# Optimization experiments

Hardware: AMD Instinct MI355X
Metric: run time of the kernel (lower is better)

The kernel has to match this reference:

```python
import jax, jax.numpy as jnp
import numpy as np

N = 50000      # nodes
E = 500000     # directed edges
F_IN = 112     # node feature dim
G = 256        # number of graphs in batch


def _lin(key, fan_in, fan_out):
    # torch nn.Linear default init: U(-1/sqrt(fan_in), 1/sqrt(fan_in))
    s = 1.0 / np.sqrt(fan_in)
    kw, kb = jax.random.split(key)
    W = jax.random.uniform(kw, (fan_in, fan_out), jnp.float32, -s, s)
    b = jax.random.uniform(kb, (fan_out,), jnp.float32, -s, s)
    return W, b


def setup_inputs() -> dict:
    key = jax.random.key(0)
    ks = jax.random.split(key, 9)
    x = jax.random.normal(ks[0], (N, F_IN), jnp.float32)
    edge_index = jax.random.randint(ks[1], (2, E), 0, N)
    # sorted graph ids, guaranteeing every graph id 0..G-1 appears
    batch = jnp.sort(jnp.concatenate([jnp.arange(G),
                                      jax.random.randint(ks[2], (N - G,), 0, G)]))
    W1, b1 = _lin(ks[3], F_IN, 336)
    W2, b2 = _lin(ks[4], 336, 168)
    Wg, bg = _lin(ks[5], 168, 84)
    Wf, bf = _lin(ks[6], 84, 42)
    Wo, bo = _lin(ks[7], 42, 1)
    return dict(x=x, edge_index=edge_index, batch=batch,
                W1=W1, b1=b1, W2=W2, b2=b2,
                Wg=Wg, bg=bg, Wf=Wf, bf=bf, Wo=Wo, bo=bo)


def _gcn_conv(x, W, b, src, dst, n):
    """PyG GCNConv: add self-loops, symmetric D^-1/2 A D^-1/2 normalization."""
    h = x @ W                                   # [n, out]
    loop = jnp.arange(n, dtype=src.dtype)
    src_f = jnp.concatenate([src, loop])        # [E+n]
    dst_f = jnp.concatenate([dst, loop])
    deg = jax.ops.segment_sum(jnp.ones(src_f.shape[0], jnp.float32), dst_f, n)
    dinv = jnp.where(deg > 0, jax.lax.rsqrt(deg), 0.0)
    norm = dinv[src_f] * dinv[dst_f]            # [E+n]
    out = jax.ops.segment_sum(h[src_f] * norm[:, None], dst_f, n)
    return out + b


def reference(x, edge_index, batch, W1, b1, W2, b2, Wg, bg, Wf, bf, Wo, bo):
    src, dst = edge_index[0], edge_index[1]
    h = jax.nn.relu(_gcn_conv(x, W1, b1, src, dst, N))
    # dropout is identity in eval mode
    h = jax.nn.relu(_gcn_conv(h, W2, b2, src, dst, N))
    g = jax.ops.segment_max(h, batch, G)        # global max pool -> [G, 168]
    g = jax.nn.relu(g @ Wg + bg)
    g = jax.nn.relu(g @ Wf + bf)
    return g @ Wo + bo                           # [G, 1]
```

## Files before the change

kernel.cpp:

```cpp
#include <hip/hip_runtime.h>
#include <hip/hip_fp16.h>

#define N_NODES 50000
#define MPAD    50048
#define N_EDGES 500000
#define F_IN    112
#define K1X     112
#define K1P     128
#define F1      336
#define K2P     352
#define F2      168
#define NGRAPH  256
#define SCAN_CHUNK 1024
#define SCAN_BLOCKS ((N_NODES + SCAN_CHUNK - 1) / SCAN_CHUNK)

typedef __attribute__((ext_vector_type(8))) _Float16 f16x8;
typedef __attribute__((ext_vector_type(4))) float f32x4;
typedef unsigned short ushort_t;

__device__ __forceinline__ ushort_t f16_bits(float x) {
    __half h = __float2half_rn(x);
    return *(ushort_t*)&h;
}

__global__ void k_zero_int(int* p, int n) {
    int i = blockIdx.x * blockDim.x + threadIdx.x;
    if (i < n) p[i] = 0;
}

#define CVX_ELEMS  (N_NODES * 28)
#define CVX_BLOCKS ((CVX_ELEMS + 255) / 256)
#define CNT_BLOCKS  ((N_EDGES / 2 + 255) / 256)
#define CVW1_BLOCKS ((384 * K1P + 255) / 256)
#define CVW2_BLOCKS ((192 * K2P + 255) / 256)
#define PREP_BLOCKS (CVX_BLOCKS + CNT_BLOCKS + CVW1_BLOCKS + CVW2_BLOCKS)

__global__ __launch_bounds__(256) void k_prep(const float* __restrict__ x,
                                              const int* __restrict__ dst,
                                              const float* __restrict__ W1,
                                              const float* __restrict__ W2,
                                              ushort_t* __restrict__ x16,
                                              int* __restrict__ dcount,
                                              ushort_t* __restrict__ w1t,
                                              ushort_t* __restrict__ w2t) {
    int bid = blockIdx.x;
    int t = threadIdx.x;
    if (bid < CVX_BLOCKS) {
        int i = bid * 256 + t;
        if (i < CVX_ELEMS) {
            float4 f = ((const float4*)x)[i];
            __half2 h0 = __floats2half2_rn(f.x, f.y);
            __half2 h1 = __floats2half2_rn(f.z, f.w);
            uint2 u; u.x = *(unsigned*)&h0; u.y = *(unsigned*)&h1;
            ((uint2*)x16)[i] = u;
        }
        return;
    }
    bid -= CVX_BLOCKS;
    if (bid < CNT_BLOCKS) {
        int i = bid * 256 + t;
        if (i < N_EDGES / 2) {
            int2 d = ((const int2*)dst)[i];
            atomicAdd(&dcount[d.x], 1);
            atomicAdd(&dcount[d.y], 1);
        }
        return;
    }
    bid -= CNT_BLOCKS;
    if (bid < CVW1_BLOCKS) {
        int idx = bid * 256 + t;
        if (idx < 384 * K1P) {
            int n = idx / K1P, k = idx % K1P;
            float v = (n < F1 && k < F_IN) ? W1[k * F1 + n] : 0.0f;
            w1t[idx] = f16_bits(v);
        }
        return;
    }
    bid -= CVW1_BLOCKS;
    {
        int idx = bid * 256 + t;
        if (idx < 192 * K2P) {
            int n = idx / K2P, k = idx % K2P;
            float v = (n < F2 && k < F1) ? W2[k * F2 + n] : 0.0f;
            w2t[idx] = f16_bits(v);
        }
    }
}

__global__ __launch_bounds__(SCAN_CHUNK) void k_scan1(const int* __restrict__ dcount,
                                                      int* __restrict__ off,
                                                      int* __restrict__ partials,
                                                      float* __restrict__ dinv, int n) {
    __shared__ int s[SCAN_CHUNK];
    int t = threadIdx.x;
    int i = blockIdx.x * SCAN_CHUNK + t;
    int val = (i < n) ? dcount[i] : 0;
    s[t] = val;
    __syncthreads();
    for (int d = 1; d < SCAN_CHUNK; d <<= 1) {
        int x = (t >= d) ? s[t - d] : 0;
        __syncthreads();
        s[t] += x;
        __syncthreads();
    }
    if (i < n) {
        off[i] = s[t] - val;
        dinv[i] = rsqrtf((float)val + 1.0f);
    }
    if (t == SCAN_CHUNK - 1) partials[blockIdx.x] = s[t];
}
__global__ __launch_bounds__(SCAN_CHUNK) void k_scan3(int* __restrict__ off,
                                                      const int* __restrict__ partials, int n) {
    __shared__ int tmp[SCAN_BLOCKS];
    __shared__ int pref[SCAN_BLOCKS];
    int t = threadIdx.x;
    if (t < SCAN_BLOCKS) tmp[t] = partials[t];
    __syncthreads();
    if (t == 0) {
        int run = 0;
        for (int j = 0; j < SCAN_BLOCKS; ++j) { pref[j] = run; run += tmp[j]; }
    }
    __syncthreads();
    int i = blockIdx.x * SCAN_CHUNK + t;
    if (i < n) off[i] += pref[blockIdx.x];
    if (i == n) off[i] = N_EDGES;
}

__global__ void k_scatter(const int* __restrict__ src, const int* __restrict__ dst,
                          const int* __restrict__ off, int* __restrict__ cur,
                          const float* __restrict__ dinv,
                          int2* __restrict__ csr, int e2) {
    int i = blockIdx.x * blockDim.x + threadIdx.x;
    if (i >= e2) return;
    int2 s2 = ((const int2*)src)[i];
    int2 d2 = ((const int2*)dst)[i];
    {
        int pos = atomicAdd(&cur[d2.x], 1);
        int2 rec; rec.x = s2.x; rec.y = __float_as_int(dinv[s2.x] * dinv[d2.x]);
        csr[off[d2.x] + pos] = rec;
    }
    {
        int pos = atomicAdd(&cur[d2.y], 1);
        int2 rec; rec.x = s2.y; rec.y = __float_as_int(dinv[s2.y] * dinv[d2.y]);
        csr[off[d2.y] + pos] = rec;
    }
}

__global__ __launch_bounds__(256) void k_agg1(const ushort_t* __restrict__ X16,
                                              const int* __restrict__ off,
                                              const int2* __restrict__ csr,
                                              const float* __restrict__ dinv,
                                              ushort_t* __restrict__ aX) {
    int w = (blockIdx.x * 256 + threadIdx.x) >> 6;
    int lane = threadIdx.x & 63;
    if (w >= N_NODES / 2) return;
    const int g = lane >> 5, sl = lane & 31;
    const int v = 2 * w + g;
    const bool act = sl < 28;
    int o0A = off[2 * w], oM = off[2 * w + 1], o1B = off[2 * w + 2];
    int o0 = g ? oM : o0A;
    int n  = g ? (o1B - oM) : (oM - o0A);
    int nmax = max(oM - o0A, o1B - oM);
    float di = dinv[v];
    float s2 = di * di;
    float4 acc = {0.f, 0.f, 0.f, 0.f};
    if (act) {
        uint2 us = *(const uint2*)(X16 + (long)v * K1X + sl * 4);
        float2 sf0 = __half22float2(*(__half2*)&us.x);
        float2 sf1 = __half22float2(*(__half2*)&us.y);
        acc.x = sf0.x * s2; acc.y = sf0.y * s2; acc.z = sf1.x * s2; acc.w = sf1.y * s2;
    }
    int nm1 = max(n - 1, 0);
    for (int b = 0; b < nmax; b += 8) {
        int2 e[8];
        #pragma unroll
        for (int j = 0; j < 8; ++j) {
            int cidx = min(o0 + min(b + j, nm1), N_EDGES - 1);
            e[j] = csr[cidx];
        }
        uint2 u[8];
        #pragma unroll
        for (int j = 0; j < 8; ++j) {
            uint2 uz; uz.x = 0u; uz.y = 0u;
            u[j] = uz;
            if (act) u[j] = *(const uint2*)(X16 + (long)e[j].x * K1X + sl * 4);
        }
        #pragma unroll
        for (int j = 0; j < 8; ++j) {
            float c = ((b + j) < n) ? __int_as_float(e[j].y) : 0.0f;
            float2 f0 = __half22float2(*(__half2*)&u[j].x);
            float2 f1 = __half22float2(*(__half2*)&u[j].y);
            acc.x += c * f0.x; acc.y += c * f0.y; acc.z += c * f1.x; acc.w += c * f1.y;
        }
    }
    __half2 h0 = __floats2half2_rn(acc.x, acc.y);
    __half2 h1 = __floats2half2_rn(acc.z, acc.w);
    uint2 o; o.x = *(unsigned*)&h0; o.y = *(unsigned*)&h1;
    *(uint2*)(aX + (long)v * K1P + sl * 4) = o;
}

__global__ __launch_bounds__(256) void k_gemm_fused(
        const ushort_t* __restrict__ aX,
        const ushort_t* __restrict__ w1t,
        const float* __restrict__ b1,
        const ushort_t* __restrict__ w2t,
        ushort_t* __restrict__ T2) {
    __shared__ ushort_t As[64][40];
    __shared__ ushort_t Bs[352][40];
    __shared__ ushort_t H1s[64][360];
    const int tid = threadIdx.x;
    const int row0 = blockIdx.x * 64;
    const int w = tid >> 6, l = tid & 63;
    const int wm = w >> 1, wn = w & 1;
    const int lm = l & 15, lq = l >> 4;

    f32x4 acc1[2][11];
    #pragma unroll
    for (int i = 0; i < 2; ++i)
        #pragma unroll
        for (int j = 0; j < 11; ++j) acc1[i][j] = (f32x4){0.f, 0.f, 0.f, 0.f};

    for (int k0 = 0; k0 < K1P; k0 += 32) {
        {
            int r = tid >> 2, s = (tid & 3) * 8;
            *(int4*)&As[r][s] = *(const int4*)&aX[(long)(row0 + r) * K1P + k0 + s];
        }
        #pragma unroll
        for (int it = 0; it < 6; ++it) {
            int f = tid + it * 256;
            if (f < 1408) {
                int r = f >> 2, s = (f & 3) * 8;
                *(int4*)&Bs[r][s] = *(const int4*)&w1t[(long)r * K1P + k0 + s];
            }
        }
        __syncthreads();
        f16x8 af0 = *(const f16x8*)&As[wm * 32 + lm][lq * 8];
        f16x8 af1 = *(const f16x8*)&As[wm * 32 + 16 + lm][lq * 8];
        #pragma unroll
        for (int ns = 0; ns < 11; ++ns) {
            f16x8 bf = *(const f16x8*)&Bs[wn * 176 + ns * 16 + lm][lq * 8];
            acc1[0][ns] = __builtin_amdgcn_mfma_f32_16x16x32_f16(af0, bf, acc1[0][ns], 0, 0, 0);
            acc1[1][ns] = __builtin_amdgcn_mfma_f32_16x16x32_f16(af1, bf, acc1[1][ns], 0, 0, 0);
        }
        __syncthreads();
    }
    #pragma unroll
    for (int ms = 0; ms < 2; ++ms)
        #pragma unroll
        for (int ns = 0; ns < 11; ++ns) {
            int col = wn * 176 + ns * 16 + lm;
            float bb = (col < F1) ? b1[col] : 0.0f;
            #pragma unroll
            for (int i = 0; i < 4; ++i) {
                int r = wm * 32 + ms * 16 + lq * 4 + i;
                H1s[r][col] = f16_bits(fmaxf(acc1[ms][ns][i] + bb, 0.0f));
            }
        }
    __syncthreads();

    f32x4 acc2[2][6];
    #pragma unroll
    for (int i = 0; i < 2; ++i)
        #pragma unroll
        for (int j = 0; j < 6; ++j) acc2[i][j] = (f32x4){0.f, 0.f, 0.f, 0.f};

    for (int k0 = 0; k0 < K2P; k0 += 32) {
        #pragma unroll
        for (int it = 0; it < 3; ++it) {
            int f = tid + it * 256;
            int r = f >> 2, s = (f & 3) * 8;
            *(int4*)&Bs[r][s] = *(const int4*)&w2t[(long)r * K2P + k0 + s];
        }
        __syncthreads();
        f16x8 af0 = *(const f16x8*)&H1s[wm * 32 + lm][k0 + lq * 8];
        f16x8 af1 = *(const f16x8*)&H1s[wm * 32 + 16 + lm][k0 + lq * 8];
        #pragma unroll
        for (int ns = 0; ns < 6; ++ns) {
            f16x8 bf = *(const f16x8*)&Bs[wn * 96 + ns * 16 + lm][lq * 8];
            acc2[0][ns] = __builtin_amdgcn_mfma_f32_16x16x32_f16(af0, bf, acc2[0][ns], 0, 0, 0);
            acc2[1][ns] = __builtin_amdgcn_mfma_f32_16x16x32_f16(af1, bf, acc2[1][ns], 0, 0, 0);
        }
        __syncthreads();
    }
    #pragma unroll
    for (int ms = 0; ms < 2; ++ms)
        #pragma unroll
        for (int ns = 0; ns < 6; ++ns) {
            int col = wn * 96 + ns * 16 + lm;
            if (col < F2) {
                #pragma unroll
                for (int i = 0; i < 4; ++i) {
                    int r = row0 + wm * 32 + ms * 16 + lq * 4 + i;
                    T2[(long)r * F2 + col] = f16_bits(acc2[ms][ns][i]);
                }
            }
        }
}

__global__ __launch_bounds__(256) void k_agg2(const ushort_t* __restrict__ T16,
                                              const int* __restrict__ off,
                                              const int2* __restrict__ csr,
                                              const float* __restrict__ dinv,
                                              const float* __restrict__ b2,
                                              const int* __restrict__ batch,
                                              float* __restrict__ gmax) {
    __shared__ __align__(16) float smax[8][168];
    __shared__ int sb[8];
    int tid = threadIdx.x;
    int w = (blockIdx.x * 256 + tid) >> 6;
    int lane = tid & 63;
    const int g = lane >> 5, sl = lane & 31;
    const int nib = tid >> 5;
    const int v = 2 * w + g;
    const bool act = sl < 21;
    int o0A = off[2 * w], oM = off[2 * w + 1], o1B = off[2 * w + 2];
    int o0 = g ? oM : o0A;
    int n  = g ? (o1B - oM) : (oM - o0A);
    int nmax = max(oM - o0A, o1B - oM);
    float di = dinv[v];
    float4 a0 = {0, 0, 0, 0}, a1 = {0, 0, 0, 0};
    if (act) {
        uint4 u = *(const uint4*)(T16 + (long)v * F2 + sl * 8);
        float2 f0 = __half22float2(*(__half2*)&u.x);
        float2 f1 = __half22float2(*(__half2*)&u.y);
        float2 f2 = __half22float2(*(__half2*)&u.z);
        float2 f3 = __half22float2(*(__half2*)&u.w);
        float s2 = di * di;
        a0.x = f0.x * s2; a0.y = f0.y * s2; a0.z = f1.x * s2; a0.w = f1.y * s2;
        a1.x = f2.x * s2; a1.y = f2.y * s2; a1.z = f3.x * s2; a1.w = f3.y * s2;
    }
    int nm1 = max(n - 1, 0);
    for (int b = 0; b < nmax; b += 8) {
        int2 e[8];
        #pragma unroll
        for (int j = 0; j < 8; ++j) {
            int cidx = min(o0 + min(b + j, nm1), N_EDGES - 1);
            e[j] = csr[cidx];
        }
        uint4 u[8];
        #pragma unroll
        for (int j = 0; j < 8; ++j) {
            int s = ((b + j) < n) ? e[j].x : v;
            if (act) u[j] = *(const uint4*)(T16 + (long)s * F2 + sl * 8);
        }
        #pragma unroll
        for (int j = 0; j < 8; ++j) {
            float c = ((b + j) < n) ? __int_as_float(e[j].y) : 0.0f;
            float2 f0 = __half22float2(*(__half2*)&u[j].x);
            float2 f1 = __half22float2(*(__half2*)&u[j].y);
            float2 f2 = __half22float2(*(__half2*)&u[j].z);
            float2 f3 = __half22float2(*(__half2*)&u[j].w);
            a0.x += c * f0.x; a0.y += c * f0.y; a0.z += c * f1.x; a0.w += c * f1.y;
            a1.x += c * f2.x; a1.y += c * f2.y; a1.z += c * f3.x; a1.w += c * f3.y;
        }
    }
    if (act) {
        float4 bb0 = ((const float4*)b2)[sl * 2];
        float4 bb1 = ((const float4*)b2)[sl * 2 + 1];
        a0.x = fmaxf(a0.x + bb0.x, 0.0f); a0.y = fmaxf(a0.y + bb0.y, 0.0f);
        a0.z = fmaxf(a0.z + bb0.z, 0.0f); a0.w = fmaxf(a0.w + bb0.w, 0.0f);
        a1.x = fmaxf(a1.x + bb1.x, 0.0f); a1.y = fmaxf(a1.y + bb1.y, 0.0f);
        a1.z = fmaxf(a1.z + bb1.z, 0.0f); a1.w = fmaxf(a1.w + bb1.w, 0.0f);
        ((float4*)&smax[nib][0])[sl * 2]     = a0;
        ((float4*)&smax[nib][0])[sl * 2 + 1] = a1;
    }
    if ((tid & 31) == 0) sb[nib] = batch[v];
    __syncthreads();
    if (tid < F2) {
        int f = tid;
        int bp = sb[0];
        float m = smax[0][f];
        #pragma unroll
        for (int r = 1; r < 8; ++r) {
            int bc = sb[r];
            float vv = smax[r][f];
            if (bc == bp) { m = fmaxf(m, vv); }
            else {
                atomicMax((int*)&gmax[bp * F2 + f], __float_as_int(m));
                m = vv; bp = bc;
            }
        }
        atomicMax((int*)&gmax[bp * F2 + f], __float_as_int(m));
    }
}

__global__ __launch_bounds__(128) void k_head(const float* __restrict__ gmax,
        const float* __restrict__ Wg, const float* __restrict__ bg,
        const float* __restrict__ Wf, const float* __restrict__ bf,
        const float* __restrict__ Wo, const float* __restrict__ bo,
        float* __restrict__ out) {
    __shared__ float s1[84];
    __shared__ float s2[42];
    int gi = blockIdx.x;
    const float* s0 = gmax + (long)gi * F2;
    int t = threadIdx.x;
    if (t < 84) {
        float acc = bg[t];
        #pragma unroll 4
        for (int k = 0; k < F2; ++k) acc += s0[k] * Wg[k * 84 + t];
        s1[t] = fmaxf(acc, 0.0f);
    }
    __syncthreads();
    if (t < 42) {
        float acc = bf[t];
        #pragma unroll 4
        for (int k = 0; k < 84; ++k) acc += s1[k] * Wf[k * 42 + t];
        s2[t] = fmaxf(acc, 0.0f);
    }
    __syncthreads();
    if (t == 0) {
        float acc = bo[0];
        for (int k = 0; k < 42; ++k) acc += s2[k] * Wo[k];
        out[gi] = acc;
    }
}

extern "C" void kernel_launch(void* const* d_in, const int* in_sizes, int n_in,
                              void* d_out, int out_size, void* d_ws, size_t ws_size,
                              hipStream_t stream) {
    const float* x   = (const float*)d_in[0];
    const int*   ei  = (const int*)d_in[1];
    const int*   bat = (const int*)d_in[2];
    const float* W1  = (const float*)d_in[3];
    const float* b1  = (const float*)d_in[4];
    const float* W2  = (const float*)d_in[5];
    const float* b2  = (const float*)d_in[6];
    const float* Wg  = (const float*)d_in[7];
    const float* bg  = (const float*)d_in[8];
    const float* Wf  = (const float*)d_in[9];
    const float* bf  = (const float*)d_in[10];
    const float* Wo  = (const float*)d_in[11];
    const float* bo  = (const float*)d_in[12];
    float* out = (float*)d_out;

    char* p = (char*)d_ws;
    float* dinv     = (float*)p; p += 50048 * 4;
    int*   dcount   = (int*)p;   p += 50048 * 4;
    int*   cur      = (int*)p;   p += 50048 * 4;
    float* gmax     = (float*)p; p += NGRAPH * F2 * 4;
    int*   off      = (int*)p;   p += 50064 * 4;
    int*   partials = (int*)p;   p += 64 * 4;
    int2*  csr      = (int2*)p;  p += (long)N_EDGES * 8;
    ushort_t* x16   = (ushort_t*)p; p += (long)N_NODES * K1X * 2;
    ushort_t* aX    = (ushort_t*)p; p += (long)MPAD * K1P * 2;
    ushort_t* w1t   = (ushort_t*)p; p += (long)384 * K1P * 2;
    ushort_t* w2t   = (ushort_t*)p; p += (long)192 * K2P * 2;
    ushort_t* t16   = (ushort_t*)p; p += (long)MPAD * F2 * 2;

    const int* src = ei;
    const int* dst = ei + N_EDGES;
    const int B = 256;
    const int ZERO_WORDS = 50048 * 2 + NGRAPH * F2;

    k_zero_int<<<(ZERO_WORDS + B - 1) / B, B, 0, stream>>>(dcount, ZERO_WORDS);
    k_prep<<<PREP_BLOCKS, B, 0, stream>>>(x, dst, W1, W2, x16, dcount, w1t, w2t);
    k_scan1<<<SCAN_BLOCKS, SCAN_CHUNK, 0, stream>>>(dcount, off, partials, dinv, N_NODES);
    k_scan3<<<SCAN_BLOCKS, SCAN_CHUNK, 0, stream>>>(off, partials, N_NODES);
    k_scatter<<<(N_EDGES / 2 + B - 1) / B, B, 0, stream>>>(src, dst, off, cur, dinv, csr, N_EDGES / 2);

    k_agg1<<<(N_NODES / 2 * 64) / 256, 256, 0, stream>>>(x16, off, csr, dinv, aX);
    k_gemm_fused<<<MPAD / 64, 256, 0, stream>>>(aX, w1t, b1, w2t, t16);

    k_agg2<<<(N_NODES / 2 * 64) / 256, 256, 0, stream>>>(t16, off, csr, dinv, b2, bat, gmax);

    k_head<<<NGRAPH, 128, 0, stream>>>(gmax, Wg, bg, Wf, bf, Wo, bo, out);
}
```

Baseline: 270.6 us.

## Assign one wavefront per node in aggregation kernels with split-edge shuffle reduction

Both aggregation kernels now map one 64-lane wavefront to a single node instead of two nodes per wave. Its edge list is split across lane groups (four quarter-waves in agg1, two half-waves in agg2), and the partial sums are combined with xor shuffles. The goal is to cut the wasted iterations that came from pairing nodes of unequal degree (the loop ran to the larger degree) and to use wider 16-byte feature loads in agg1. In exchange it launches more waves, adds shuffle reductions, and for short edge lists leaves some lane groups idle with padded loads.

```diff
diff --git a/kernel.cpp b/kernel.cpp
--- a/kernel.cpp
+++ b/kernel.cpp
@@ -146,57 +146,75 @@
     }
 }
 
-__global__ __launch_bounds__(256) void k_agg1(const ushort_t* __restrict__ X16,
-                                              const int* __restrict__ off,
-                                              const int2* __restrict__ csr,
-                                              const float* __restrict__ dinv,
-                                              ushort_t* __restrict__ aX) {
-    int w = (blockIdx.x * 256 + threadIdx.x) >> 6;
-    int lane = threadIdx.x & 63;
-    if (w >= N_NODES / 2) return;
-    const int g = lane >> 5, sl = lane & 31;
-    const int v = 2 * w + g;
-    const bool act = sl < 28;
-    int o0A = off[2 * w], oM = off[2 * w + 1], o1B = off[2 * w + 2];
-    int o0 = g ? oM : o0A;
-    int n  = g ? (o1B - oM) : (oM - o0A);
-    int nmax = max(oM - o0A, o1B - oM);
-    float di = dinv[v];
-    float s2 = di * di;
-    float4 acc = {0.f, 0.f, 0.f, 0.f};
-    if (act) {
-        uint2 us = *(const uint2*)(X16 + (long)v * K1X + sl * 4);
-        float2 sf0 = __half22float2(*(__half2*)&us.x);
-        float2 sf1 = __half22float2(*(__half2*)&us.y);
-        acc.x = sf0.x * s2; acc.y = sf0.y * s2; acc.z = sf1.x * s2; acc.w = sf1.y * s2;
-    }
-    int nm1 = max(n - 1, 0);
-    for (int b = 0; b < nmax; b += 8) {
+__global__ __launch_bounds__(256, 4) void k_agg1(const ushort_t* __restrict__ X16,
+                                                 const int* __restrict__ off,
+                                                 const int2* __restrict__ csr,
+                                                 const float* __restrict__ dinv,
+                                                 ushort_t* __restrict__ aX) {
+    const int wid = (blockIdx.x * 256 + threadIdx.x) >> 6;
+    const int lane = threadIdx.x & 63;
+    const int q = lane >> 4, ql = lane & 15;
+    const bool act = ql < 14;
+    const int v = wid;
+    const int o0 = off[v], o1 = off[v + 1];
+    const int n = o1 - o0;
+    const float di = dinv[v];
+    float4 aL = {0, 0, 0, 0}, aH = {0, 0, 0, 0};
+    if (act && q == 0) {
+        uint4 u = *(const uint4*)(X16 + (long)v * K1X + ql * 8);
+        float s2 = di * di;
+        float2 f0 = __half22float2(*(__half2*)&u.x);
+        float2 f1 = __half22float2(*(__half2*)&u.y);
+        float2 f2 = __half22float2(*(__half2*)&u.z);
+        float2 f3 = __half22float2(*(__half2*)&u.w);
+        aL.x = f0.x * s2; aL.y = f0.y * s2; aL.z = f1.x * s2; aL.w = f1.y * s2;
+        aH.x = f2.x * s2; aH.y = f2.y * s2; aH.z = f3.x * s2; aH.w = f3.y * s2;
+    }
+    const int nm1 = max(n - 1, 0);
+    for (int b = q * 8; b < n; b += 32) {
         int2 e[8];
         #pragma unroll
         for (int j = 0; j < 8; ++j) {
             int cidx = min(o0 + min(b + j, nm1), N_EDGES - 1);
             e[j] = csr[cidx];
         }
-        uint2 u[8];
-        #pragma unroll
-        for (int j = 0; j < 8; ++j) {
-            uint2 uz; uz.x = 0u; uz.y = 0u;
+        uint4 u[8];
+        #pragma unroll
+        for (int j = 0; j < 8; ++j) {
+            uint4 uz = {0u, 0u, 0u, 0u};
             u[j] = uz;
-            if (act) u[j] = *(const uint2*)(X16 + (long)e[j].x * K1X + sl * 4);
+            if (act) u[j] = *(const uint4*)(X16 + (long)e[j].x * K1X + ql * 8);
         }
         #pragma unroll
         for (int j = 0; j < 8; ++j) {
             float c = ((b + j) < n) ? __int_as_float(e[j].y) : 0.0f;
             float2 f0 = __half22float2(*(__half2*)&u[j].x);
             float2 f1 = __half22float2(*(__half2*)&u[j].y);
-            acc.x += c * f0.x; acc.y += c * f0.y; acc.z += c * f1.x; acc.w += c * f1.y;
-        }
-    }
-    __half2 h0 = __floats2half2_rn(acc.x, acc.y);
-    __half2 h1 = __floats2half2_rn(acc.z, acc.w);
-    uint2 o; o.x = *(unsigned*)&h0; o.y = *(unsigned*)&h1;
-    *(uint2*)(aX + (long)v * K1P + sl * 4) = o;
+            float2 f2 = __half22float2(*(__half2*)&u[j].z);
+            float2 f3 = __half22float2(*(__half2*)&u[j].w);
+            aL.x += c * f0.x; aL.y += c * f0.y; aL.z += c * f1.x; aL.w += c * f1.y;
+            aH.x += c * f2.x; aH.y += c * f2.y; aH.z += c * f3.x; aH.w += c * f3.y;
+        }
+    }
+    aL.x += __shfl_xor(aL.x, 16); aL.y += __shfl_xor(aL.y, 16);
+    aL.z += __shfl_xor(aL.z, 16); aL.w += __shfl_xor(aL.w, 16);
+    aH.x += __shfl_xor(aH.x, 16); aH.y += __shfl_xor(aH.y, 16);
+    aH.z += __shfl_xor(aH.z, 16); aH.w += __shfl_xor(aH.w, 16);
+    aL.x += __shfl_xor(aL.x, 32); aL.y += __shfl_xor(aL.y, 32);
+    aL.z += __shfl_xor(aL.z, 32); aL.w += __shfl_xor(aL.w, 32);
+    aH.x += __shfl_xor(aH.x, 32); aH.y += __shfl_xor(aH.y, 32);
+    aH.z += __shfl_xor(aH.z, 32); aH.w += __shfl_xor(aH.w, 32);
+    if (q == 0) {
+        __half2 h0 = __floats2half2_rn(aL.x, aL.y);
+        __half2 h1 = __floats2half2_rn(aL.z, aL.w);
+        __half2 h2 = __floats2half2_rn(aH.x, aH.y);
+        __half2 h3 = __floats2half2_rn(aH.z, aH.w);
+        uint4 o;
+        o.x = *(unsigned*)&h0; o.y = *(unsigned*)&h1;
+        o.z = *(unsigned*)&h2; o.w = *(unsigned*)&h3;
+        if (!act) { o.x = 0; o.y = 0; o.z = 0; o.w = 0; }
+        *(uint4*)(aX + (long)v * K1P + ql * 8) = o;
+    }
 }
 
 __global__ __launch_bounds__(256) void k_gemm_fused(
@@ -297,30 +315,27 @@
         }
 }
 
-__global__ __launch_bounds__(256) void k_agg2(const ushort_t* __restrict__ T16,
-                                              const int* __restrict__ off,
-                                              const int2* __restrict__ csr,
-                                              const float* __restrict__ dinv,
-                                              const float* __restrict__ b2,
-                                              const int* __restrict__ batch,
-                                              float* __restrict__ gmax) {
+__global__ __launch_bounds__(512, 4) void k_agg2(const ushort_t* __restrict__ T16,
+                                                 const int* __restrict__ off,
+                                                 const int2* __restrict__ csr,
+                                                 const float* __restrict__ dinv,
+                                                 const float* __restrict__ b2,
+                                                 const int* __restrict__ batch,
+                                                 float* __restrict__ gmax) {
     __shared__ __align__(16) float smax[8][168];
     __shared__ int sb[8];
-    int tid = threadIdx.x;
-    int w = (blockIdx.x * 256 + tid) >> 6;
-    int lane = tid & 63;
-    const int g = lane >> 5, sl = lane & 31;
-    const int nib = tid >> 5;
-    const int v = 2 * w + g;
-    const bool act = sl < 21;
-    int o0A = off[2 * w], oM = off[2 * w + 1], o1B = off[2 * w + 2];
-    int o0 = g ? oM : o0A;
-    int n  = g ? (o1B - oM) : (oM - o0A);
-    int nmax = max(oM - o0A, o1B - oM);
-    float di = dinv[v];
+    const int tid = threadIdx.x;
+    const int wv = tid >> 6;
+    const int lane = tid & 63;
+    const int h = lane >> 5, hl = lane & 31;
+    const bool act = hl < 21;
+    const int v = blockIdx.x * 8 + wv;
+    const int o0 = off[v], o1 = off[v + 1];
+    const int n = o1 - o0;
+    const float di = dinv[v];
     float4 a0 = {0, 0, 0, 0}, a1 = {0, 0, 0, 0};
-    if (act) {
-        uint4 u = *(const uint4*)(T16 + (long)v * F2 + sl * 8);
+    if (act && h == 0) {
+        uint4 u = *(const uint4*)(T16 + (long)v * F2 + hl * 8);
         float2 f0 = __half22float2(*(__half2*)&u.x);
         float2 f1 = __half22float2(*(__half2*)&u.y);
         float2 f2 = __half22float2(*(__half2*)&u.z);
@@ -329,8 +344,8 @@
         a0.x = f0.x * s2; a0.y = f0.y * s2; a0.z = f1.x * s2; a0.w = f1.y * s2;
         a1.x = f2.x * s2; a1.y = f2.y * s2; a1.z = f3.x * s2; a1.w = f3.y * s2;
     }
-    int nm1 = max(n - 1, 0);
-    for (int b = 0; b < nmax; b += 8) {
+    const int nm1 = max(n - 1, 0);
+    for (int b = h * 8; b < n; b += 16) {
         int2 e[8];
         #pragma unroll
         for (int j = 0; j < 8; ++j) {
@@ -340,8 +355,9 @@
         uint4 u[8];
         #pragma unroll
         for (int j = 0; j < 8; ++j) {
-            int s = ((b + j) < n) ? e[j].x : v;
-            if (act) u[j] = *(const uint4*)(T16 + (long)s * F2 + sl * 8);
+            uint4 uz = {0u, 0u, 0u, 0u};
+            u[j] = uz;
+            if (act) u[j] = *(const uint4*)(T16 + (long)e[j].x * F2 + hl * 8);
         }
         #pragma unroll
         for (int j = 0; j < 8; ++j) {
@@ -354,17 +370,21 @@
             a1.x += c * f2.x; a1.y += c * f2.y; a1.z += c * f3.x; a1.w += c * f3.y;
         }
     }
-    if (act) {
-        float4 bb0 = ((const float4*)b2)[sl * 2];
-        float4 bb1 = ((const float4*)b2)[sl * 2 + 1];
+    a0.x += __shfl_xor(a0.x, 32); a0.y += __shfl_xor(a0.y, 32);
+    a0.z += __shfl_xor(a0.z, 32); a0.w += __shfl_xor(a0.w, 32);
+    a1.x += __shfl_xor(a1.x, 32); a1.y += __shfl_xor(a1.y, 32);
+    a1.z += __shfl_xor(a1.z, 32); a1.w += __shfl_xor(a1.w, 32);
+    if (act && h == 0) {
+        float4 bb0 = ((const float4*)b2)[hl * 2];
+        float4 bb1 = ((const float4*)b2)[hl * 2 + 1];
         a0.x = fmaxf(a0.x + bb0.x, 0.0f); a0.y = fmaxf(a0.y + bb0.y, 0.0f);
         a0.z = fmaxf(a0.z + bb0.z, 0.0f); a0.w = fmaxf(a0.w + bb0.w, 0.0f);
         a1.x = fmaxf(a1.x + bb1.x, 0.0f); a1.y = fmaxf(a1.y + bb1.y, 0.0f);
         a1.z = fmaxf(a1.z + bb1.z, 0.0f); a1.w = fmaxf(a1.w + bb1.w, 0.0f);
-        ((float4*)&smax[nib][0])[sl * 2]     = a0;
-        ((float4*)&smax[nib][0])[sl * 2 + 1] = a1;
-    }
-    if ((tid & 31) == 0) sb[nib] = batch[v];
+        ((float4*)&smax[wv][0])[hl * 2]     = a0;
+        ((float4*)&smax[wv][0])[hl * 2 + 1] = a1;
+    }
+    if (lane == 0) sb[wv] = batch[v];
     __syncthreads();
     if (tid < F2) {
         int f = tid;
@@ -458,10 +478,10 @@
     k_scan3<<<SCAN_BLOCKS, SCAN_CHUNK, 0, stream>>>(off, partials, N_NODES);
     k_scatter<<<(N_EDGES / 2 + B - 1) / B, B, 0, stream>>>(src, dst, off, cur, dinv, csr, N_EDGES / 2);
 
-    k_agg1<<<(N_NODES / 2 * 64) / 256, 256, 0, stream>>>(x16, off, csr, dinv, aX);
+    k_agg1<<<N_NODES / 4, 256, 0, stream>>>(x16, off, csr, dinv, aX);
     k_gemm_fused<<<MPAD / 64, 256, 0, stream>>>(aX, w1t, b1, w2t, t16);
 
-    k_agg2<<<(N_NODES / 2 * 64) / 256, 256, 0, stream>>>(t16, off, csr, dinv, b2, bat, gmax);
+    k_agg2<<<N_NODES / 8, 512, 0, stream>>>(t16, off, csr, dinv, b2, bat, gmax);
 
     k_head<<<NGRAPH, 128, 0, stream>>>(gmax, Wg, bg, Wf, bf, Wo, bo, out);
 }
```

New measurement: 292.7 us. 8.2% more time.
